# Kernel optimization log

Measured on AMD Instinct MI355X. Metric: run time of the kernel, lower is better.

The kernel has to match this reference:

```python
import jax, jax.numpy as jnp
import numpy as np

D_MODEL = 1024
NUM_HEADS = 16
HEAD_DIM = D_MODEL // NUM_HEADS


def setup_inputs() -> dict:
    key = jax.random.key(0)
    ks = jax.random.split(key, 11)
    B, S, D = 2, 2048, D_MODEL
    s = 1.0 / np.sqrt(D)
    return {
        "query": jax.random.normal(ks[0], (B, S, D), jnp.float32),
        "key": jax.random.normal(ks[1], (B, S, D), jnp.float32),
        "value": jax.random.normal(ks[2], (B, S, D), jnp.float32),
        "W_q": jax.random.normal(ks[3], (D, D), jnp.float32) * s,
        "b_q": jnp.zeros((D,), jnp.float32),
        "W_k": jax.random.normal(ks[4], (D, D), jnp.float32) * s,
        "b_k": jnp.zeros((D,), jnp.float32),
        "W_v": jax.random.normal(ks[5], (D, D), jnp.float32) * s,
        "b_v": jnp.zeros((D,), jnp.float32),
        "W_o": jax.random.normal(ks[6], (D, D), jnp.float32) * s,
        "b_o": jnp.zeros((D,), jnp.float32),
    }


def reference(query, key, value, W_q, b_q, W_k, b_k, W_v, b_v, W_o, b_o):
    B, S, D = query.shape
    H, Dh = NUM_HEADS, HEAD_DIM
    # linear projections then split heads: [B, S, D] -> [B, H, S, Dh]
    def split_heads(x):
        return x.reshape(B, -1, H, Dh).transpose(0, 2, 1, 3)
    Q = split_heads(query @ W_q.T + b_q)
    K = split_heads(key @ W_k.T + b_k)
    V = split_heads(value @ W_v.T + b_v)
    # NOTE: original scales by d_model**-0.5, not head_dim**-0.5
    scale = jnp.asarray(D, Q.dtype) ** -0.5
    scores = jnp.einsum("bhqd,bhkd->bhqk", Q, K) * scale
    attn = jax.nn.softmax(scores, axis=-1)  # includes max-subtraction stabilization
    out = jnp.einsum("bhqk,bhkd->bhqd", attn, V)
    out = out.transpose(0, 2, 1, 3).reshape(B, -1, D)
    return out @ W_o.T + b_o
```

## Files before the change

### kernel.cpp

```cpp
#include <hip/hip_runtime.h>
#include <stdint.h>


typedef unsigned short u16;
typedef short s16x8 __attribute__((ext_vector_type(8)));
typedef short s16x4 __attribute__((ext_vector_type(4)));
typedef float f32x4 __attribute__((ext_vector_type(4)));
typedef u16 u16x4 __attribute__((ext_vector_type(4)));

#define S_LEN 2048
#define DMODEL 1024
#define LOG2E 1.44269504088896340736f

__device__ __forceinline__ u16 f2bf(float f) {
  union { float f; uint32_t u; } v; v.f = f;
  return (u16)((v.u + 0x8000u) >> 16);
}

__device__ __forceinline__ s16x8 ld8f(const float* s) {
  f32x4 a = *(const f32x4*)s;
  f32x4 b = *(const f32x4*)(s + 4);
  s16x8 r;
  r[0] = (short)f2bf(a[0]); r[1] = (short)f2bf(a[1]);
  r[2] = (short)f2bf(a[2]); r[3] = (short)f2bf(a[3]);
  r[4] = (short)f2bf(b[0]); r[5] = (short)f2bf(b[1]);
  r[6] = (short)f2bf(b[2]); r[7] = (short)f2bf(b[3]);
  return r;
}

__device__ __forceinline__ void gl2lds16(const u16* g, u16* l) {
  __builtin_amdgcn_global_load_lds(
      (const __attribute__((address_space(1))) uint32_t*)g,
      (__attribute__((address_space(3))) uint32_t*)l, 16, 0, 0);
}

struct Cvt7 { const float* s[7]; u16* d[7]; int n[7]; };

__global__ __launch_bounds__(256) void cvt7(Cvt7 p) {
  const int z = blockIdx.y;
  const int idx = blockIdx.x * 256 + threadIdx.x;
  if (idx * 8 < p.n[z])
    *(s16x8*)(p.d[z] + (size_t)idx * 8) = ld8f(p.s[z] + (size_t)idx * 8);
}

struct GemmBatch {
  const u16* A[3]; const u16* W[3]; const float* Bv[3]; void* C[3];
  u16* vt;
  float scl[3];
};

template <int BM, int BN, bool OUT_F32, bool VT>
__global__ __launch_bounds__(256) void gemm_bt(GemmBatch p, int M, int N, int K) {
  static_assert(!VT || (BM == 128 && BN == 128), "VT epilogue assumes 128x128");
  constexpr int MI = BM / 32, NJ = BN / 32;
  constexpr int TS = BM + 8;
  constexpr int AB = BM * 64 + BN * 64;
  constexpr int TB = VT ? BN * TS : 0;
  constexpr int SM = AB > TB ? AB : TB;
  __shared__ u16 smem[SM];
  u16* const As = smem;
  u16* const Ws = smem + BM * 64;

  const int z = blockIdx.z;
  const u16* __restrict__ A      = p.A[z];
  const u16* __restrict__ W      = p.W[z];
  const float* __restrict__ bias = p.Bv[z];
  const float scl = p.scl[z];

  const int tid = threadIdx.x;
  const int wave = tid >> 6, lane = tid & 63;
  const int quad = lane >> 4, l16 = lane & 15;
  const int bm = blockIdx.y * BM, bn = blockIdx.x * BN;
  const int wr = (wave >> 1) * (BM / 2), wc = (wave & 1) * (BN / 2);
  const int sr8 = lane >> 3;
  const int slc = (lane & 7) ^ sr8;
  const int srow = wave * 8 + sr8;

  f32x4 acc[MI][NJ];
#pragma unroll
  for (int i = 0; i < MI; i++)
#pragma unroll
    for (int j = 0; j < NJ; j++) acc[i][j] = {0.f, 0.f, 0.f, 0.f};

  const u16* Ab = A + (size_t)bm * K;
  const u16* Wb = W + (size_t)bn * K;

  for (int kt = 0; kt < K; kt += 64) {
    __syncthreads();
#pragma unroll
    for (int i = 0; i < MI; i++)
      gl2lds16(Ab + (size_t)(i * 32 + srow) * K + kt + slc * 8,
               &As[(i * 32 + wave * 8) * 64]);
#pragma unroll
    for (int i = 0; i < NJ; i++)
      gl2lds16(Wb + (size_t)(i * 32 + srow) * K + kt + slc * 8,
               &Ws[(i * 32 + wave * 8) * 64]);
    __syncthreads();

#pragma unroll
    for (int ks = 0; ks < 2; ks++) {
      const int ch = ks * 4 + quad;
      s16x8 a[MI], b[NJ];
#pragma unroll
      for (int t = 0; t < MI; t++)
        a[t] = *(const s16x8*)&As[(wr + t * 16 + l16) * 64 + ((ch ^ (l16 & 7)) << 3)];
#pragma unroll
      for (int t = 0; t < NJ; t++)
        b[t] = *(const s16x8*)&Ws[(wc + t * 16 + l16) * 64 + ((ch ^ (l16 & 7)) << 3)];
#pragma unroll
      for (int i = 0; i < MI; i++)
#pragma unroll
        for (int j = 0; j < NJ; j++)
          acc[i][j] = __builtin_amdgcn_mfma_f32_16x16x32_bf16(a[i], b[j], acc[i][j], 0, 0, 0);
    }
  }

  if (VT && z == 2) {
    __syncthreads();
    u16* const T = smem;
#pragma unroll
    for (int j = 0; j < NJ; j++) {
      const int c = wc + j * 16 + l16;
      const float bv = bias[bn + c];
#pragma unroll
      for (int i = 0; i < MI; i++) {
        const int r0 = wr + i * 16 + quad * 4;
        u16x4 t4;
#pragma unroll
        for (int r = 0; r < 4; r++) t4[r] = f2bf((acc[i][j][r] + bv) * scl);
        *(u16x4*)&T[c * TS + r0] = t4;
      }
    }
    __syncthreads();
    const int c = tid >> 1, half = tid & 1;
    const int b_ = bm >> 11;
    const int sb = (bm & 2047) + half * 64;
    u16* dst = p.vt + (size_t)(b_ * 1024 + bn + c) * S_LEN + sb;
    const u16* srcT = &T[c * TS + half * 64];
#pragma unroll
    for (int k = 0; k < 8; k++)
      *(s16x8*)(dst + k * 8) = *(const s16x8*)(srcT + k * 8);
  } else {
#pragma unroll
    for (int j = 0; j < NJ; j++) {
      const int col = bn + wc + j * 16 + l16;
      const float bv = bias[col];
#pragma unroll
      for (int i = 0; i < MI; i++) {
        const int row0 = bm + wr + i * 16 + quad * 4;
#pragma unroll
        for (int r = 0; r < 4; r++) {
          const float val = (acc[i][j][r] + bv) * scl;
          if (OUT_F32)
            ((float*)p.C[z])[(size_t)(row0 + r) * N + col] = val;
          else
            ((u16*)p.C[z])[(size_t)(row0 + r) * N + col] = f2bf(val);
        }
      }
    }
  }
}

__global__ __launch_bounds__(512, 2) void attn_kernel(const u16* __restrict__ Qp,
                                                      const u16* __restrict__ Kp,
                                                      const u16* __restrict__ Vt,
                                                      u16* __restrict__ AO) {
  __shared__ u16 Qs[128 * 64];
  __shared__ u16 Ks[128 * 64];
  __shared__ u16 Vs[64 * 128];

  const int tid = threadIdx.x;
  const int wave = tid >> 6, lane = tid & 63;
  const int quad = lane >> 4, l16 = lane & 15;
  const int bh = blockIdx.y, b = bh >> 4, h = bh & 15;
  const int s0 = blockIdx.x * 128;

  const int sr = tid >> 3, sc8 = tid & 7;
  const int sxor = (sc8 ^ (sr & 7)) << 3;
  const int vr = tid >> 4, vc = tid & 15;
  const int vxor = (vc ^ (vr & 15)) << 3;

#pragma unroll
  for (int i = 0; i < 2; i++) {
    const int rr = i * 64 + sr;
    s16x8 qv = *(const s16x8*)(Qp + (size_t)(b * S_LEN + s0 + rr) * DMODEL + h * 64 + sc8 * 8);
    *(s16x8*)&Qs[rr * 64 + sxor] = qv;
  }
  __syncthreads();

  s16x8 aq[2];
#pragma unroll
  for (int ks = 0; ks < 2; ks++) {
    const int ch = ks * 4 + quad;
    aq[ks] = *(const s16x8*)&Qs[(wave * 16 + l16) * 64 + ((ch ^ (l16 & 7)) << 3)];
  }

  s16x8 kv[2], vv[2];
#pragma unroll
  for (int i = 0; i < 2; i++)
    kv[i] = *(const s16x8*)(Kp + (size_t)(b * S_LEN + i * 64 + sr) * DMODEL + h * 64 + sc8 * 8);
#pragma unroll
  for (int i = 0; i < 2; i++)
    vv[i] = *(const s16x8*)(Vt + (size_t)(bh * 64 + i * 32 + vr) * S_LEN + vc * 8);

  f32x4 o[4];
  float l_r = 0.f;
#pragma unroll
  for (int dt = 0; dt < 4; dt++) o[dt] = {0.f, 0.f, 0.f, 0.f};

  const f32x4 zf = {0.f, 0.f, 0.f, 0.f};

  for (int kt = 0; kt < S_LEN; kt += 128) {
    __syncthreads();
#pragma unroll
    for (int i = 0; i < 2; i++)
      *(s16x8*)&Ks[(i * 64 + sr) * 64 + sxor] = kv[i];
#pragma unroll
    for (int i = 0; i < 2; i++)
      *(s16x8*)&Vs[(i * 32 + vr) * 128 + vxor] = vv[i];
    __syncthreads();

    if (kt + 128 < S_LEN) {
      const int k2 = kt + 128;
#pragma unroll
      for (int i = 0; i < 2; i++)
        kv[i] = *(const s16x8*)(Kp + (size_t)(b * S_LEN + k2 + i * 64 + sr) * DMODEL + h * 64 + sc8 * 8);
#pragma unroll
      for (int i = 0; i < 2; i++)
        vv[i] = *(const s16x8*)(Vt + (size_t)(bh * 64 + i * 32 + vr) * S_LEN + k2 + vc * 8);
    }

#pragma unroll
    for (int kvt = 0; kvt < 8; kvt++) {
      const int krow = kvt * 16 + l16;
      s16x8 ak0 = *(const s16x8*)&Ks[krow * 64 + (((0 + quad) ^ (l16 & 7)) << 3)];
      s16x8 ak1 = *(const s16x8*)&Ks[krow * 64 + (((4 + quad) ^ (l16 & 7)) << 3)];
      f32x4 sA;
      sA = __builtin_amdgcn_mfma_f32_16x16x32_bf16(ak0, aq[0], zf, 0, 0, 0);
      sA = __builtin_amdgcn_mfma_f32_16x16x32_bf16(ak1, aq[1], sA, 0, 0, 0);

      union { float f; uint32_t u; } e0, e1, e2, e3;
      e0.f = __builtin_amdgcn_exp2f(sA[0]);
      e1.f = __builtin_amdgcn_exp2f(sA[1]);
      e2.f = __builtin_amdgcn_exp2f(sA[2]);
      e3.f = __builtin_amdgcn_exp2f(sA[3]);
      l_r += (((e0.f + e1.f) + e2.f) + e3.f);

      union { uint32_t u[2]; s16x4 v; } pk;
      pk.u[0] = __builtin_amdgcn_perm(e1.u + 0x8000u, e0.u + 0x8000u, 0x07060302u);
      pk.u[1] = __builtin_amdgcn_perm(e3.u + 0x8000u, e2.u + 0x8000u, 0x07060302u);
      const s16x4 pf = pk.v;

      const int ch = kvt * 2 + (quad >> 1);
#pragma unroll
      for (int dt = 0; dt < 4; dt++) {
        const int row = dt * 16 + l16;
        s16x4 bv = *(const s16x4*)&Vs[row * 128 + ((ch ^ l16) << 3) + (quad & 1) * 4];
        o[dt] = __builtin_amdgcn_mfma_f32_16x16x16bf16_1k(pf, bv, o[dt], 0, 0, 0);
      }
    }
  }

  l_r += __shfl_xor(l_r, 16);
  l_r += __shfl_xor(l_r, 32);
#pragma unroll
  for (int r = 0; r < 4; r++) {
    const float linv = 1.f / __shfl(l_r, quad * 4 + r);
    const int row = s0 + wave * 16 + quad * 4 + r;
#pragma unroll
    for (int dt = 0; dt < 4; dt++)
      AO[(size_t)(b * S_LEN + row) * DMODEL + h * 64 + dt * 16 + l16] =
          f2bf(o[dt][r] * linv);
  }
}

extern "C" void kernel_launch(void* const* d_in, const int* in_sizes, int n_in,
                              void* d_out, int out_size, void* d_ws, size_t ws_size,
                              hipStream_t stream) {
  const float* query = (const float*)d_in[0];
  const float* key_  = (const float*)d_in[1];
  const float* value = (const float*)d_in[2];
  const float* W_q = (const float*)d_in[3];
  const float* b_q = (const float*)d_in[4];
  const float* W_k = (const float*)d_in[5];
  const float* b_k = (const float*)d_in[6];
  const float* W_v = (const float*)d_in[7];
  const float* b_v = (const float*)d_in[8];
  const float* W_o = (const float*)d_in[9];
  const float* b_o = (const float*)d_in[10];
  float* out = (float*)d_out;

  const int M = 2 * S_LEN;
  const int N = DMODEL, K = DMODEL;
  const size_t WSZ = (size_t)DMODEL * DMODEL;
  const size_t SZ  = (size_t)M * DMODEL;

  u16* Wqb = (u16*)d_ws;
  u16* Wkb = Wqb + WSZ;
  u16* Wvb = Wkb + WSZ;
  u16* Wob = Wvb + WSZ;
  u16* Qa  = Wob + WSZ;
  u16* Ka  = Qa + SZ;
  u16* Va  = Ka + SZ;
  u16* Qp  = Va + SZ;
  u16* Kp  = Qp + SZ;
  u16* Vt  = Kp + SZ;
  u16* AO  = Qp;

  Cvt7 cw;
  cw.s[0] = W_q;   cw.d[0] = Wqb; cw.n[0] = (int)WSZ;
  cw.s[1] = W_k;   cw.d[1] = Wkb; cw.n[1] = (int)WSZ;
  cw.s[2] = W_v;   cw.d[2] = Wvb; cw.n[2] = (int)WSZ;
  cw.s[3] = W_o;   cw.d[3] = Wob; cw.n[3] = (int)WSZ;
  cw.s[4] = query; cw.d[4] = Qa;  cw.n[4] = (int)SZ;
  cw.s[5] = key_;  cw.d[5] = Ka;  cw.n[5] = (int)SZ;
  cw.s[6] = value; cw.d[6] = Va;  cw.n[6] = (int)SZ;
  cvt7<<<dim3((int)(SZ / 2048), 7), 256, 0, stream>>>(cw);

  GemmBatch p1;
  p1.A[0] = Qa; p1.W[0] = Wqb; p1.Bv[0] = b_q; p1.C[0] = Qp;
  p1.A[1] = Ka; p1.W[1] = Wkb; p1.Bv[1] = b_k; p1.C[1] = Kp;
  p1.A[2] = Va; p1.W[2] = Wvb; p1.Bv[2] = b_v; p1.C[2] = Vt;
  p1.vt = Vt;
  p1.scl[0] = 0.03125f * LOG2E;
  p1.scl[1] = 1.0f;
  p1.scl[2] = 1.0f;
  gemm_bt<128, 128, false, true><<<dim3(N / 128, M / 128, 3), 256, 0, stream>>>(p1, M, N, K);

  attn_kernel<<<dim3(S_LEN / 128, 32), 512, 0, stream>>>(Qp, Kp, Vt, AO);

  GemmBatch p2;
  p2.A[0] = AO; p2.W[0] = Wob; p2.Bv[0] = b_o; p2.C[0] = out;
  p2.A[1] = AO; p2.W[1] = Wob; p2.Bv[1] = b_o; p2.C[1] = out;
  p2.A[2] = AO; p2.W[2] = Wob; p2.Bv[2] = b_o; p2.C[2] = out;
  p2.vt = nullptr;
  p2.scl[0] = 1.0f; p2.scl[1] = 1.0f; p2.scl[2] = 1.0f;
  gemm_bt<64, 64, true, false><<<dim3(N / 64, M / 64, 1), 256, 0, stream>>>(p2, M, N, K);
}
```

Baseline: 229.3 us.

## Split KV tile across wave halves with 32 query rows per wave and merge

Each wave now handles 32 query rows (two 16-row tiles) against half of each 128-key tile, with waves 0-3 and 4-7 splitting the keys. Each K fragment loaded from LDS is reused by two score MFMAs and each V fragment by two PV MFMAs, which halves LDS reads per MFMA. The partial O and row-sum results of the two wave halves are merged through shared memory at the end. Launch bounds occupancy rises from 2 to 4 blocks per CU, which tightens the register budget while each wave now holds more accumulators, so spilling is a risk.

```diff
diff --git a/kernel.cpp b/kernel.cpp
--- a/kernel.cpp
+++ b/kernel.cpp
@@ -161,19 +161,22 @@
   }
 }
 
-__global__ __launch_bounds__(512, 2) void attn_kernel(const u16* __restrict__ Qp,
+__global__ __launch_bounds__(512, 4) void attn_kernel(const u16* __restrict__ Qp,
                                                       const u16* __restrict__ Kp,
                                                       const u16* __restrict__ Vt,
                                                       u16* __restrict__ AO) {
-  __shared__ u16 Qs[128 * 64];
-  __shared__ u16 Ks[128 * 64];
-  __shared__ u16 Vs[64 * 128];
+  __shared__ u16 smem[24576];
+  u16* const Qs = smem;
+  u16* const Ks = smem + 8192;
+  u16* const Vs = smem + 16384;
 
   const int tid = threadIdx.x;
   const int wave = tid >> 6, lane = tid & 63;
   const int quad = lane >> 4, l16 = lane & 15;
   const int bh = blockIdx.y, b = bh >> 4, h = bh & 15;
   const int s0 = blockIdx.x * 128;
+  const int qw = wave & 3;
+  const int kvh = wave >> 2;
 
   const int sr = tid >> 3, sc8 = tid & 7;
   const int sxor = (sc8 ^ (sr & 7)) << 3;
@@ -188,12 +191,15 @@
   }
   __syncthreads();
 
-  s16x8 aq[2];
-#pragma unroll
-  for (int ks = 0; ks < 2; ks++) {
-    const int ch = ks * 4 + quad;
-    aq[ks] = *(const s16x8*)&Qs[(wave * 16 + l16) * 64 + ((ch ^ (l16 & 7)) << 3)];
-  }
+  s16x8 aq[2][2];
+#pragma unroll
+  for (int ks = 0; ks < 2; ks++)
+#pragma unroll
+    for (int rt = 0; rt < 2; rt++) {
+      const int row = qw * 32 + rt * 16 + l16;
+      const int ch = ks * 4 + quad;
+      aq[ks][rt] = *(const s16x8*)&Qs[row * 64 + ((ch ^ (l16 & 7)) << 3)];
+    }
 
   s16x8 kv[2], vv[2];
 #pragma unroll
@@ -203,10 +209,12 @@
   for (int i = 0; i < 2; i++)
     vv[i] = *(const s16x8*)(Vt + (size_t)(bh * 64 + i * 32 + vr) * S_LEN + vc * 8);
 
-  f32x4 o[4];
-  float l_r = 0.f;
-#pragma unroll
-  for (int dt = 0; dt < 4; dt++) o[dt] = {0.f, 0.f, 0.f, 0.f};
+  f32x4 o[2][4];
+  float l_r[2] = {0.f, 0.f};
+#pragma unroll
+  for (int rt = 0; rt < 2; rt++)
+#pragma unroll
+    for (int dt = 0; dt < 4; dt++) o[rt][dt] = {0.f, 0.f, 0.f, 0.f};
 
   const f32x4 zf = {0.f, 0.f, 0.f, 0.f};
 
@@ -231,46 +239,84 @@
     }
 
 #pragma unroll
-    for (int kvt = 0; kvt < 8; kvt++) {
-      const int krow = kvt * 16 + l16;
+    for (int kvt = 0; kvt < 4; kvt++) {
+      const int krow = kvh * 64 + kvt * 16 + l16;
       s16x8 ak0 = *(const s16x8*)&Ks[krow * 64 + (((0 + quad) ^ (l16 & 7)) << 3)];
       s16x8 ak1 = *(const s16x8*)&Ks[krow * 64 + (((4 + quad) ^ (l16 & 7)) << 3)];
-      f32x4 sA;
-      sA = __builtin_amdgcn_mfma_f32_16x16x32_bf16(ak0, aq[0], zf, 0, 0, 0);
-      sA = __builtin_amdgcn_mfma_f32_16x16x32_bf16(ak1, aq[1], sA, 0, 0, 0);
-
-      union { float f; uint32_t u; } e0, e1, e2, e3;
-      e0.f = __builtin_amdgcn_exp2f(sA[0]);
-      e1.f = __builtin_amdgcn_exp2f(sA[1]);
-      e2.f = __builtin_amdgcn_exp2f(sA[2]);
-      e3.f = __builtin_amdgcn_exp2f(sA[3]);
-      l_r += (((e0.f + e1.f) + e2.f) + e3.f);
-
-      union { uint32_t u[2]; s16x4 v; } pk;
-      pk.u[0] = __builtin_amdgcn_perm(e1.u + 0x8000u, e0.u + 0x8000u, 0x07060302u);
-      pk.u[1] = __builtin_amdgcn_perm(e3.u + 0x8000u, e2.u + 0x8000u, 0x07060302u);
-      const s16x4 pf = pk.v;
-
-      const int ch = kvt * 2 + (quad >> 1);
+
+      s16x4 pf[2];
+#pragma unroll
+      for (int rt = 0; rt < 2; rt++) {
+        f32x4 sA;
+        sA = __builtin_amdgcn_mfma_f32_16x16x32_bf16(ak0, aq[0][rt], zf, 0, 0, 0);
+        sA = __builtin_amdgcn_mfma_f32_16x16x32_bf16(ak1, aq[1][rt], sA, 0, 0, 0);
+
+        union { float f; uint32_t u; } e0, e1, e2, e3;
+        e0.f = __builtin_amdgcn_exp2f(sA[0]);
+        e1.f = __builtin_amdgcn_exp2f(sA[1]);
+        e2.f = __builtin_amdgcn_exp2f(sA[2]);
+        e3.f = __builtin_amdgcn_exp2f(sA[3]);
+        l_r[rt] += (((e0.f + e1.f) + e2.f) + e3.f);
+
+        union { uint32_t u[2]; s16x4 v; } pk;
+        pk.u[0] = __builtin_amdgcn_perm(e1.u + 0x8000u, e0.u + 0x8000u, 0x07060302u);
+        pk.u[1] = __builtin_amdgcn_perm(e3.u + 0x8000u, e2.u + 0x8000u, 0x07060302u);
+        pf[rt] = pk.v;
+      }
+
+      const int ch = kvh * 8 + kvt * 2 + (quad >> 1);
 #pragma unroll
       for (int dt = 0; dt < 4; dt++) {
         const int row = dt * 16 + l16;
         s16x4 bv = *(const s16x4*)&Vs[row * 128 + ((ch ^ l16) << 3) + (quad & 1) * 4];
-        o[dt] = __builtin_amdgcn_mfma_f32_16x16x16bf16_1k(pf, bv, o[dt], 0, 0, 0);
-      }
-    }
-  }
-
-  l_r += __shfl_xor(l_r, 16);
-  l_r += __shfl_xor(l_r, 32);
-#pragma unroll
-  for (int r = 0; r < 4; r++) {
-    const float linv = 1.f / __shfl(l_r, quad * 4 + r);
-    const int row = s0 + wave * 16 + quad * 4 + r;
-#pragma unroll
-    for (int dt = 0; dt < 4; dt++)
-      AO[(size_t)(b * S_LEN + row) * DMODEL + h * 64 + dt * 16 + l16] =
-          f2bf(o[dt][r] * linv);
+        o[0][dt] = __builtin_amdgcn_mfma_f32_16x16x16bf16_1k(pf[0], bv, o[0][dt], 0, 0, 0);
+        o[1][dt] = __builtin_amdgcn_mfma_f32_16x16x16bf16_1k(pf[1], bv, o[1][dt], 0, 0, 0);
+      }
+    }
+  }
+
+#pragma unroll
+  for (int rt = 0; rt < 2; rt++) {
+    l_r[rt] += __shfl_xor(l_r[rt], 16);
+    l_r[rt] += __shfl_xor(l_r[rt], 32);
+  }
+
+  __syncthreads();
+  f32x4* const mrgO = (f32x4*)smem;
+  float* const mrgL = (float*)smem + 8192;
+  if (wave >= 4) {
+    const int w = wave - 4;
+#pragma unroll
+    for (int rt = 0; rt < 2; rt++) {
+#pragma unroll
+      for (int dt = 0; dt < 4; dt++)
+        mrgO[(rt * 4 + dt) * 256 + w * 64 + lane] = o[rt][dt];
+      mrgL[rt * 256 + w * 64 + lane] = l_r[rt];
+    }
+  }
+  __syncthreads();
+  if (wave < 4) {
+#pragma unroll
+    for (int rt = 0; rt < 2; rt++) {
+#pragma unroll
+      for (int dt = 0; dt < 4; dt++) {
+        f32x4 ov = mrgO[(rt * 4 + dt) * 256 + wave * 64 + lane];
+        o[rt][dt] += ov;
+      }
+      l_r[rt] += mrgL[rt * 256 + wave * 64 + lane];
+    }
+#pragma unroll
+    for (int rt = 0; rt < 2; rt++) {
+#pragma unroll
+      for (int r = 0; r < 4; r++) {
+        const float linv = 1.f / __shfl(l_r[rt], quad * 4 + r);
+        const int row = s0 + qw * 32 + rt * 16 + quad * 4 + r;
+#pragma unroll
+        for (int dt = 0; dt < 4; dt++)
+          AO[(size_t)(b * S_LEN + row) * DMODEL + h * 64 + dt * 16 + l16] =
+              f2bf(o[rt][dt][r] * linv);
+      }
+    }
   }
 }
 
```

Result: no change. 227.8 us (-0.6%).
